# Optimization experiments

Measured on AMD Instinct MI355X. Metric: run time of the kernel, lower is better.

## Reference

```python
import jax, jax.numpy as jnp
import numpy as np

B, D = 4096, 128
TEMPERATURE = 0.2

def setup_inputs() -> dict:
    key = jax.random.key(0)
    k1, k2 = jax.random.split(key)
    z1 = jax.random.normal(k1, (B, D), dtype=jnp.float32)
    z2 = jax.random.normal(k2, (B, D), dtype=jnp.float32)
    return {"z1": z1, "z2": z2}

def reference(z1, z2):
    # single-process path: global batch == local batch
    gb = z1.shape[0]
    z = jnp.concatenate([z1, z2], axis=0)              # [2B, D]
    sim = jnp.matmul(z, z.T) / TEMPERATURE             # [2B, 2B]
    n = 2 * gb
    diag = jnp.eye(n, dtype=bool)
    sim = jnp.where(diag, jnp.finfo(sim.dtype).min, sim)
    targets = jnp.concatenate([jnp.arange(gb, n), jnp.arange(0, gb)])
    logp = jax.nn.log_softmax(sim, axis=-1)            # [2B, 2B]
    loss_all = -logp[jnp.arange(n), targets]           # [2B]
    # rank 0, world_size 1 -> idx_keep covers all rows
    return loss_all.mean()
```

## Files before the change

### kernel.cpp

```cpp
#include <hip/hip_runtime.h>
#include <stdint.h>

typedef unsigned short u16;
typedef unsigned int u32;

#define NTOT 8192
#define BH   4096
#define DD   128
#define COLSPLIT 8
#define COLS_PER_SPLIT (NTOT / COLSPLIT)
#define TILE_COLS 128
#define TILES_PER_SPLIT (COLS_PER_SPLIT / TILE_COLS)
#define ROWS_PER_BLOCK 128
#define LDS_PITCH 136
#define NEG_INF (-3.0e38f)
#define SCALE_IN 2.68579144f
#define LN2F 0.6931471805599453f

typedef __bf16 bf16x8 __attribute__((ext_vector_type(8)));
typedef float  f32x4  __attribute__((ext_vector_type(4)));

__device__ __forceinline__ u16 f2bf(float f) {
  u32 u = __float_as_uint(f);
  return (u16)((u + 0x7fffu + ((u >> 16) & 1u)) >> 16);
}

__device__ __forceinline__ float fexp2(float x) {
#if __has_builtin(__builtin_amdgcn_exp2f)
  return __builtin_amdgcn_exp2f(x);
#else
  float r; asm("v_exp_f32 %0, %1" : "=v"(r) : "v"(x)); return r;
#endif
}

__global__ __launch_bounds__(256) void ntx_convert(
    const float* __restrict__ z1, const float* __restrict__ z2,
    u16* __restrict__ zb, float* __restrict__ out) {
  if (blockIdx.x == 0 && threadIdx.x == 0) out[0] = 0.f;
  const int i = (blockIdx.x * 256 + threadIdx.x) * 4;
  const int half = BH * DD;
  float4 v = (i < half) ? *reinterpret_cast<const float4*>(z1 + i)
                        : *reinterpret_cast<const float4*>(z2 + (i - half));
  u32 lo = (u32)f2bf(v.x * SCALE_IN) | ((u32)f2bf(v.y * SCALE_IN) << 16);
  u32 hi = (u32)f2bf(v.z * SCALE_IN) | ((u32)f2bf(v.w * SCALE_IN) << 16);
  uint2 o; o.x = lo; o.y = hi;
  *reinterpret_cast<uint2*>(zb + i) = o;
}

__global__ __launch_bounds__(256, 2) void ntx_main(
    const u16* __restrict__ zb,
    float* __restrict__ m_part, float* __restrict__ l_part,
    float* __restrict__ st_part) {
  __shared__ u16 lds_tile[TILE_COLS * LDS_PITCH];

  const int tid  = threadIdx.x;
  const int wave = tid >> 6;
  const int lane = tid & 63;
  const int l15  = lane & 15;
  const int q    = lane >> 4;

  const int rowhalf = wave & 1;
  const int colhalf = wave >> 1;
  const int cwl     = colhalf * 64;

  const int rwave = blockIdx.x * ROWS_PER_BLOCK + rowhalf * 64;
  const int split = blockIdx.y;
  const int col0  = split * COLS_PER_SPLIT;

  bf16x8 afrag[4][4];
#pragma unroll
  for (int rt = 0; rt < 4; ++rt)
#pragma unroll
    for (int kk = 0; kk < 4; ++kk) {
      const int r = rwave + rt * 16 + l15;
      afrag[rt][kk] = *reinterpret_cast<const bf16x8*>(zb + r * DD + kk * 32 + q * 8);
    }

  float m_run[4][4], l_run[4][4], stv[4][4];
#pragma unroll
  for (int rt = 0; rt < 4; ++rt)
#pragma unroll
    for (int r = 0; r < 4; ++r) { m_run[rt][r] = NEG_INF; l_run[rt][r] = 0.f; stv[rt][r] = NEG_INF; }

  for (int t = 0; t < TILES_PER_SPLIT; ++t) {
    const int ct0 = col0 + t * TILE_COLS;

    __syncthreads();
    {
      const uint4* src = reinterpret_cast<const uint4*>(zb + ct0 * DD);
#pragma unroll
      for (int i = 0; i < 8; ++i) {
        const int c   = tid + i * 256;
        const int col = c >> 4, w16 = c & 15;
        uint4 v = src[c];
        *reinterpret_cast<uint4*>(lds_tile + col * LDS_PITCH + w16 * 8) = v;
      }
    }
    __syncthreads();

    f32x4 acc[4][4];
#pragma unroll
    for (int rt = 0; rt < 4; ++rt)
#pragma unroll
      for (int cs = 0; cs < 4; ++cs) acc[rt][cs] = (f32x4){0.f, 0.f, 0.f, 0.f};

#pragma unroll
    for (int cs = 0; cs < 4; ++cs) {
      bf16x8 bfrag[4];
#pragma unroll
      for (int kk = 0; kk < 4; ++kk)
        bfrag[kk] = *reinterpret_cast<const bf16x8*>(
            lds_tile + (cwl + cs * 16 + l15) * LDS_PITCH + kk * 32 + q * 8);
#pragma unroll
      for (int rt = 0; rt < 4; ++rt)
#pragma unroll
        for (int kk = 0; kk < 4; ++kk)
          acc[rt][cs] = __builtin_amdgcn_mfma_f32_16x16x32_bf16(
              afrag[rt][kk], bfrag[kk], acc[rt][cs], 0, 0, 0);
    }

    const int  ccol0    = ct0 + cwl;
    const bool has_diag = (ccol0 == rwave);
    const bool has_tgt  = (ccol0 == (rwave ^ BH));
    if (has_diag || has_tgt) {
#pragma unroll
      for (int rt = 0; rt < 4; ++rt)
#pragma unroll
        for (int r = 0; r < 4; ++r) {
          const int grow = rwave + rt * 16 + q * 4 + r;
#pragma unroll
          for (int cs = 0; cs < 4; ++cs) {
            const int gcol = ccol0 + cs * 16 + l15;
            float v = acc[rt][cs][r];
            if (gcol == (grow ^ BH)) stv[rt][r] = fmaxf(stv[rt][r], v);
            if (gcol == grow) acc[rt][cs][r] = NEG_INF;
          }
        }
    }

#pragma unroll
    for (int rt = 0; rt < 4; ++rt)
#pragma unroll
      for (int r = 0; r < 4; ++r) {
        float mx = acc[rt][0][r];
#pragma unroll
        for (int cs = 1; cs < 4; ++cs) mx = fmaxf(mx, acc[rt][cs][r]);
        const float mnew = fmaxf(m_run[rt][r], mx);
        float s = 0.f;
#pragma unroll
        for (int cs = 0; cs < 4; ++cs) s += fexp2(acc[rt][cs][r] - mnew);
        l_run[rt][r] = l_run[rt][r] * fexp2(m_run[rt][r] - mnew) + s;
        m_run[rt][r] = mnew;
      }
  }

#pragma unroll
  for (int rt = 0; rt < 4; ++rt)
#pragma unroll
    for (int r = 0; r < 4; ++r) {
      float m = m_run[rt][r], l = l_run[rt][r];
#pragma unroll
      for (int off = 1; off < 16; off <<= 1) {
        const float mo = __shfl_xor(m, off, 64);
        const float lo = __shfl_xor(l, off, 64);
        const float mn = fmaxf(m, mo);
        l = l * fexp2(m - mn) + lo * fexp2(mo - mn);
        m = mn;
      }
      float sv = stv[rt][r];
#pragma unroll
      for (int off = 1; off < 16; off <<= 1) sv = fmaxf(sv, __shfl_xor(sv, off, 64));
      if (l15 == 0) {
        const int grow = rwave + rt * 16 + q * 4 + r;
        const int sp   = split * 2 + colhalf;
        m_part[sp * NTOT + grow] = m;
        l_part[sp * NTOT + grow] = l;
        const int tcol = grow ^ BH;
        if (tcol >= col0 && tcol < col0 + COLS_PER_SPLIT &&
            (((tcol >> 6) & 1) == colhalf))
          st_part[grow] = sv;
      }
    }
}

__global__ __launch_bounds__(256) void ntx_finish(
    const float* __restrict__ m_part, const float* __restrict__ l_part,
    const float* __restrict__ st_part, float* __restrict__ out) {
  const int row = blockIdx.x * 256 + threadIdx.x;
  float m = NEG_INF;
#pragma unroll
  for (int s = 0; s < COLSPLIT * 2; ++s) m = fmaxf(m, m_part[s * NTOT + row]);
  float l = 0.f;
#pragma unroll
  for (int s = 0; s < COLSPLIT * 2; ++s)
    l += l_part[s * NTOT + row] * fexp2(m_part[s * NTOT + row] - m);
  float loss = LN2F * (m + __log2f(l) - st_part[row]);

#pragma unroll
  for (int off = 32; off >= 1; off >>= 1) loss += __shfl_xor(loss, off, 64);
  __shared__ float wsum[4];
  if ((threadIdx.x & 63) == 0) wsum[threadIdx.x >> 6] = loss;
  __syncthreads();
  if (threadIdx.x == 0) {
    float s = wsum[0] + wsum[1] + wsum[2] + wsum[3];
    atomicAdd(out, s * (1.0f / NTOT));
  }
}

extern "C" void kernel_launch(void* const* d_in, const int* in_sizes, int n_in,
                              void* d_out, int out_size, void* d_ws, size_t ws_size,
                              hipStream_t stream) {
  const float* z1 = (const float*)d_in[0];
  const float* z2 = (const float*)d_in[1];
  float* out = (float*)d_out;

  char* ws = (char*)d_ws;
  u16*   zb      = (u16*)ws;
  float* m_part  = (float*)(ws + (size_t)NTOT * DD * 2);
  float* l_part  = m_part + COLSPLIT * 2 * NTOT;
  float* st_part = l_part + COLSPLIT * 2 * NTOT;

  ntx_convert<<<dim3((NTOT * DD) / (256 * 4)), dim3(256), 0, stream>>>(z1, z2, zb, out);
  ntx_main<<<dim3(NTOT / ROWS_PER_BLOCK, COLSPLIT), dim3(256), 0, stream>>>(
      zb, m_part, l_part, st_part);
  ntx_finish<<<dim3(NTOT / 256), dim3(256), 0, stream>>>(m_part, l_part, st_part, out);
}
```

Before: 90.85 us.

## Drop LDS staging and load B fragments directly from global per wave

Each wave now covers 64 rows across the whole column split and reads its B fragments in 32-column chunks straight from global memory, with no LDS tile and no __syncthreads. This removes the barrier and LDS round trip, and the grid changes to 256-row blocks with 16 column splits. The cost is that the four waves of a block each fetch the same B data separately, leaning on L1/L2 for reuse. Online-softmax updates now run every 32 columns instead of every 64, which adds rescale exp work per MFMA.

```diff
diff --git a/kernel.cpp b/kernel.cpp
--- a/kernel.cpp
+++ b/kernel.cpp
@@ -7,12 +7,8 @@
 #define NTOT 8192
 #define BH   4096
 #define DD   128
-#define COLSPLIT 8
-#define COLS_PER_SPLIT (NTOT / COLSPLIT)
-#define TILE_COLS 128
-#define TILES_PER_SPLIT (COLS_PER_SPLIT / TILE_COLS)
-#define ROWS_PER_BLOCK 128
-#define LDS_PITCH 136
+#define NSPLIT 16
+#define COLS_PER_SPLIT (NTOT / NSPLIT)
 #define NEG_INF (-3.0e38f)
 #define SCALE_IN 2.68579144f
 #define LN2F 0.6931471805599453f
@@ -51,19 +47,13 @@
     const u16* __restrict__ zb,
     float* __restrict__ m_part, float* __restrict__ l_part,
     float* __restrict__ st_part) {
-  __shared__ u16 lds_tile[TILE_COLS * LDS_PITCH];
-
   const int tid  = threadIdx.x;
   const int wave = tid >> 6;
   const int lane = tid & 63;
   const int l15  = lane & 15;
   const int q    = lane >> 4;
 
-  const int rowhalf = wave & 1;
-  const int colhalf = wave >> 1;
-  const int cwl     = colhalf * 64;
-
-  const int rwave = blockIdx.x * ROWS_PER_BLOCK + rowhalf * 64;
+  const int rwave = blockIdx.x * 256 + wave * 64;
   const int split = blockIdx.y;
   const int col0  = split * COLS_PER_SPLIT;
 
@@ -82,55 +72,42 @@
 #pragma unroll
     for (int r = 0; r < 4; ++r) { m_run[rt][r] = NEG_INF; l_run[rt][r] = 0.f; stv[rt][r] = NEG_INF; }
 
-  for (int t = 0; t < TILES_PER_SPLIT; ++t) {
-    const int ct0 = col0 + t * TILE_COLS;
+  for (int it = 0; it < COLS_PER_SPLIT / 32; ++it) {
+    const int cb = col0 + it * 32;
 
-    __syncthreads();
-    {
-      const uint4* src = reinterpret_cast<const uint4*>(zb + ct0 * DD);
+    bf16x8 bfrag[2][4];
 #pragma unroll
-      for (int i = 0; i < 8; ++i) {
-        const int c   = tid + i * 256;
-        const int col = c >> 4, w16 = c & 15;
-        uint4 v = src[c];
-        *reinterpret_cast<uint4*>(lds_tile + col * LDS_PITCH + w16 * 8) = v;
-      }
-    }
-    __syncthreads();
+    for (int cs = 0; cs < 2; ++cs)
+#pragma unroll
+      for (int kk = 0; kk < 4; ++kk)
+        bfrag[cs][kk] = *reinterpret_cast<const bf16x8*>(
+            zb + (cb + cs * 16 + l15) * DD + kk * 32 + q * 8);
 
-    f32x4 acc[4][4];
+    f32x4 acc[4][2];
 #pragma unroll
     for (int rt = 0; rt < 4; ++rt)
 #pragma unroll
-      for (int cs = 0; cs < 4; ++cs) acc[rt][cs] = (f32x4){0.f, 0.f, 0.f, 0.f};
+      for (int cs = 0; cs < 2; ++cs) acc[rt][cs] = (f32x4){0.f, 0.f, 0.f, 0.f};
 
 #pragma unroll
-    for (int cs = 0; cs < 4; ++cs) {
-      bf16x8 bfrag[4];
-#pragma unroll
-      for (int kk = 0; kk < 4; ++kk)
-        bfrag[kk] = *reinterpret_cast<const bf16x8*>(
-            lds_tile + (cwl + cs * 16 + l15) * LDS_PITCH + kk * 32 + q * 8);
+    for (int cs = 0; cs < 2; ++cs)
 #pragma unroll
       for (int rt = 0; rt < 4; ++rt)
 #pragma unroll
         for (int kk = 0; kk < 4; ++kk)
           acc[rt][cs] = __builtin_amdgcn_mfma_f32_16x16x32_bf16(
-              afrag[rt][kk], bfrag[kk], acc[rt][cs], 0, 0, 0);
-    }
+              afrag[rt][kk], bfrag[cs][kk], acc[rt][cs], 0, 0, 0);
 
-    const int  ccol0    = ct0 + cwl;
-    const bool has_diag = (ccol0 == rwave);
-    const bool has_tgt  = (ccol0 == (rwave ^ BH));
-    if (has_diag || has_tgt) {
+    const int cb64 = cb & ~63;
+    if (cb64 == rwave || cb64 == (rwave ^ BH)) {
 #pragma unroll
       for (int rt = 0; rt < 4; ++rt)
 #pragma unroll
         for (int r = 0; r < 4; ++r) {
           const int grow = rwave + rt * 16 + q * 4 + r;
 #pragma unroll
-          for (int cs = 0; cs < 4; ++cs) {
-            const int gcol = ccol0 + cs * 16 + l15;
+          for (int cs = 0; cs < 2; ++cs) {
+            const int gcol = cb + cs * 16 + l15;
             float v = acc[rt][cs][r];
             if (gcol == (grow ^ BH)) stv[rt][r] = fmaxf(stv[rt][r], v);
             if (gcol == grow) acc[rt][cs][r] = NEG_INF;
@@ -142,13 +119,9 @@
     for (int rt = 0; rt < 4; ++rt)
 #pragma unroll
       for (int r = 0; r < 4; ++r) {
-        float mx = acc[rt][0][r];
-#pragma unroll
-        for (int cs = 1; cs < 4; ++cs) mx = fmaxf(mx, acc[rt][cs][r]);
-        const float mnew = fmaxf(m_run[rt][r], mx);
-        float s = 0.f;
-#pragma unroll
-        for (int cs = 0; cs < 4; ++cs) s += fexp2(acc[rt][cs][r] - mnew);
+        const float a0 = acc[rt][0][r], a1 = acc[rt][1][r];
+        const float mnew = fmaxf(m_run[rt][r], fmaxf(a0, a1));
+        const float s = fexp2(a0 - mnew) + fexp2(a1 - mnew);
         l_run[rt][r] = l_run[rt][r] * fexp2(m_run[rt][r] - mnew) + s;
         m_run[rt][r] = mnew;
       }
@@ -172,13 +145,10 @@
       for (int off = 1; off < 16; off <<= 1) sv = fmaxf(sv, __shfl_xor(sv, off, 64));
       if (l15 == 0) {
         const int grow = rwave + rt * 16 + q * 4 + r;
-        const int sp   = split * 2 + colhalf;
-        m_part[sp * NTOT + grow] = m;
-        l_part[sp * NTOT + grow] = l;
+        m_part[split * NTOT + grow] = m;
+        l_part[split * NTOT + grow] = l;
         const int tcol = grow ^ BH;
-        if (tcol >= col0 && tcol < col0 + COLS_PER_SPLIT &&
-            (((tcol >> 6) & 1) == colhalf))
-          st_part[grow] = sv;
+        if ((tcol >> 9) == split) st_part[grow] = sv;
       }
     }
 }
@@ -189,10 +159,10 @@
   const int row = blockIdx.x * 256 + threadIdx.x;
   float m = NEG_INF;
 #pragma unroll
-  for (int s = 0; s < COLSPLIT * 2; ++s) m = fmaxf(m, m_part[s * NTOT + row]);
+  for (int s = 0; s < NSPLIT; ++s) m = fmaxf(m, m_part[s * NTOT + row]);
   float l = 0.f;
 #pragma unroll
-  for (int s = 0; s < COLSPLIT * 2; ++s)
+  for (int s = 0; s < NSPLIT; ++s)
     l += l_part[s * NTOT + row] * fexp2(m_part[s * NTOT + row] - m);
   float loss = LN2F * (m + __log2f(l) - st_part[row]);
 
@@ -217,11 +187,11 @@
   char* ws = (char*)d_ws;
   u16*   zb      = (u16*)ws;
   float* m_part  = (float*)(ws + (size_t)NTOT * DD * 2);
-  float* l_part  = m_part + COLSPLIT * 2 * NTOT;
-  float* st_part = l_part + COLSPLIT * 2 * NTOT;
+  float* l_part  = m_part + NSPLIT * NTOT;
+  float* st_part = l_part + NSPLIT * NTOT;
 
   ntx_convert<<<dim3((NTOT * DD) / (256 * 4)), dim3(256), 0, stream>>>(z1, z2, zb, out);
-  ntx_main<<<dim3(NTOT / ROWS_PER_BLOCK, COLSPLIT), dim3(256), 0, stream>>>(
+  ntx_main<<<dim3(NTOT / 256, NSPLIT), dim3(256), 0, stream>>>(
       zb, m_part, l_part, st_part);
   ntx_finish<<<dim3(NTOT / 256), dim3(256), 0, stream>>>(m_part, l_part, st_part, out);
 }
```

Result: slower. 103.1 us (+13.5%).
